# Optimization experiments

Hardware: AMD Instinct MI355X
Metric: run time of the kernel (lower is better)

The kernel has to match this reference:

```python
import jax, jax.numpy as jnp
import numpy as np

N_NODES = 10000
N_EDGES = 320000
NODE_F = 64
EDGE_F = 32
H = 256
L = 6
HEADS = 8
OUT = H // HEADS
N_GRAPHS = 16
NEG_SLOPE = 0.2  # PyG GATConv leaky_relu slope


def setup_inputs() -> dict:
    key = jax.random.key(0)
    ks = jax.random.split(key, 32)
    s = 0.05
    f32 = jnp.float32
    inp = {}
    inp["x"] = jax.random.normal(ks[0], (N_NODES, NODE_F), f32)
    inp["edge_index"] = jax.random.randint(ks[1], (2, N_EDGES), 0, N_NODES)
    inp["edge_attr"] = jax.random.normal(ks[2], (N_EDGES, EDGE_F), f32)
    inp["batch"] = jnp.sort(jax.random.randint(ks[3], (N_NODES,), 0, N_GRAPHS))
    # embeddings
    inp["node_w"] = jax.random.normal(ks[4], (H, NODE_F), f32) * s
    inp["node_b"] = jnp.zeros((H,), f32)
    inp["edge_emb_w"] = jax.random.normal(ks[5], (H, EDGE_F), f32) * s
    inp["edge_emb_b"] = jnp.zeros((H,), f32)
    # stacked GATConv params (shared lin for src/dst since in_channels is int)
    inp["lin_w"] = jax.random.normal(ks[6], (L, H, H), f32) * s
    inp["att_src"] = jax.random.normal(ks[7], (L, HEADS, OUT), f32) * s
    inp["att_dst"] = jax.random.normal(ks[8], (L, HEADS, OUT), f32) * s
    inp["att_edge"] = jax.random.normal(ks[9], (L, HEADS, OUT), f32) * s
    inp["lin_edge_w"] = jax.random.normal(ks[10], (L, H, H), f32) * s
    inp["conv_b"] = jnp.zeros((L, H), f32)
    inp["ln_g"] = jnp.ones((L, H), f32)
    inp["ln_b"] = jnp.zeros((L, H), f32)
    # MLP heads: Linear(2H->H), Linear(H->H/2), Linear(H/2->3)
    inp["pw1"] = jax.random.normal(ks[11], (H, 2 * H), f32) * s
    inp["pb1"] = jnp.zeros((H,), f32)
    inp["pw2"] = jax.random.normal(ks[12], (H // 2, H), f32) * s
    inp["pb2"] = jnp.zeros((H // 2,), f32)
    inp["pw3"] = jax.random.normal(ks[13], (3, H // 2), f32) * s
    inp["pb3"] = jnp.zeros((3,), f32)
    inp["mw1"] = jax.random.normal(ks[14], (H, 2 * H), f32) * s
    inp["mb1"] = jnp.zeros((H,), f32)
    inp["mw2"] = jax.random.normal(ks[15], (H // 2, H), f32) * s
    inp["mb2"] = jnp.zeros((H // 2,), f32)
    inp["mw3"] = jax.random.normal(ks[16], (3, H // 2), f32) * s
    inp["mb3"] = jnp.zeros((3,), f32)
    return inp


def _ln(x, g, b):
    mu = jnp.mean(x, -1, keepdims=True)
    var = jnp.mean(jnp.square(x - mu), -1, keepdims=True)
    return g * (x - mu) * jax.lax.rsqrt(var + 1e-5) + b


def _mlp(z, w1, b1, w2, b2, w3, b3):
    h = jax.nn.gelu(z @ w1.T + b1, approximate=False)
    h = jax.nn.gelu(h @ w2.T + b2, approximate=False)
    return jax.nn.sigmoid(h @ w3.T + b3)


def _gnn_forward(x, edge_attr, src, dst, batch,
                 node_w, node_b, edge_emb_w, edge_emb_b,
                 lin_w, att_src, att_dst, att_edge, lin_edge_w, conv_b,
                 ln_g, ln_b,
                 pw1, pb1, pw2, pb2, pw3, pb3,
                 mw1, mb1, mw2, mb2, mw3, mb3):
    h = x @ node_w.T + node_b                       # [N, H]
    ea = edge_attr @ edge_emb_w.T + edge_emb_b      # [E, H]
    # PyG add_self_loops(fill_value='mean'): loop attr = mean of incoming edge attrs
    cnt = jax.ops.segment_sum(jnp.ones((N_EDGES,), h.dtype), dst, N_NODES)
    loop_attr = jax.ops.segment_sum(ea, dst, N_NODES) / jnp.maximum(cnt, 1.0)[:, None]
    ea_full = jnp.concatenate([ea, loop_attr], 0)   # [E+N, H]
    loops = jnp.arange(N_NODES, dtype=src.dtype)
    src_f = jnp.concatenate([src, loops])
    dst_f = jnp.concatenate([dst, loops])
    for i in range(L):
        x_in = h
        xw = (h @ lin_w[i].T).reshape(N_NODES, HEADS, OUT)
        eap = (ea_full @ lin_edge_w[i].T).reshape(-1, HEADS, OUT)
        a_src = jnp.sum(xw * att_src[i], -1)        # [N, heads]
        a_dst = jnp.sum(xw * att_dst[i], -1)
        alpha = a_src[src_f] + a_dst[dst_f] + jnp.sum(eap * att_edge[i], -1)  # [E+N, heads]
        alpha = jnp.where(alpha > 0, alpha, NEG_SLOPE * alpha)
        amax = jax.ops.segment_max(alpha, dst_f, N_NODES)
        e = jnp.exp(alpha - amax[dst_f])
        denom = jax.ops.segment_sum(e, dst_f, N_NODES)
        w = e / (denom[dst_f] + 1e-16)
        msg = xw[src_f] * w[:, :, None]             # [E+N, heads, out]
        hi = jax.ops.segment_sum(msg, dst_f, N_NODES).reshape(N_NODES, H) + conv_b[i]
        hi = jax.nn.gelu(_ln(hi, ln_g[i], ln_b[i]), approximate=False)
        h = hi + x_in if i > 0 else hi
    sums = jax.ops.segment_sum(h, batch, N_GRAPHS)  # [G, H]
    ncnt = jax.ops.segment_sum(jnp.ones((N_NODES,), h.dtype), batch, N_GRAPHS)
    mean = sums / jnp.maximum(ncnt, 1.0)[:, None]
    xg = jnp.concatenate([mean, sums], 1)           # [G, 2H]
    params = _mlp(xg, pw1, pb1, pw2, pb2, pw3, pb3)
    metrics = _mlp(xg, mw1, mb1, mw2, mb2, mw3, mb3)
    return params, metrics


def reference(x, edge_index, edge_attr, batch,
              node_w, node_b, edge_emb_w, edge_emb_b,
              lin_w, att_src, att_dst, att_edge, lin_edge_w, conv_b,
              ln_g, ln_b,
              pw1, pb1, pw2, pb2, pw3, pb3,
              mw1, mb1, mw2, mb2, mw3, mb3):
    return _gnn_forward(x, edge_attr, edge_index[0], edge_index[1], batch,
                        node_w, node_b, edge_emb_w, edge_emb_b,
                        lin_w, att_src, att_dst, att_edge, lin_edge_w, conv_b,
                        ln_g, ln_b,
                        pw1, pb1, pw2, pb2, pw3, pb3,
                        mw1, mb1, mw2, mb2, mw3, mb3)
```

## Files before the change

### kernel.cpp

```cpp
#include <hip/hip_runtime.h>
#include <math.h>

#define NN 10000
#define NE 320000
#define NODE_F 64
#define EDGE_F 32
#define HDIM 256
#define HEADS 8
#define LAYERS 6
#define NG 16
#define NOUT 48
#define LOG2E 1.4426950408889634f

typedef __attribute__((ext_vector_type(8))) short short8;
typedef __attribute__((ext_vector_type(4))) float float4v;
typedef __attribute__((ext_vector_type(2))) float floatx2;

__global__ void scan_kernel(const int* __restrict__ cnt, int* __restrict__ row_ptr,
                            int* __restrict__ pos) {
    __shared__ int wsum[16];
    __shared__ int woff[16];
    int t = threadIdx.x;
    int lane = t & 63, wid = t >> 6;
    const int chunk = 10;
    int lo = t * chunk;
    int loc[10];
    int s = 0;
    #pragma unroll
    for (int k = 0; k < 10; ++k) {
        int i = lo + k;
        int v = (i < NN) ? cnt[i] : 0;
        loc[k] = v;
        s += v;
    }
    int inc = s;
    #pragma unroll
    for (int off = 1; off < 64; off <<= 1) {
        int v = __shfl_up(inc, off, 64);
        if (lane >= off) inc += v;
    }
    if (lane == 63) wsum[wid] = inc;
    __syncthreads();
    if (t < 16) {
        int inc2 = wsum[t];
        #pragma unroll
        for (int off = 1; off < 16; off <<= 1) {
            int u = __shfl_up(inc2, off, 16);
            if (t >= off) inc2 += u;
        }
        woff[t] = inc2;
    }
    __syncthreads();
    int base = inc - s + (wid ? woff[wid - 1] : 0);
    #pragma unroll
    for (int k = 0; k < 10; ++k) {
        int i = lo + k;
        if (i < NN) {
            row_ptr[i] = base;
            pos[i] = base;
            base += loc[k];
        }
    }
    if (t == 1023) row_ptr[NN] = woff[15];
}

__global__ void scatter_kernel(const int* __restrict__ src, const int* __restrict__ dst,
                               int* __restrict__ pos, int2* __restrict__ csr_se) {
    int e = blockIdx.x * 256 + threadIdx.x;
    if (e >= NE) return;
    int d = dst[e];
    int idx = atomicAdd(&pos[d], 1);
    csr_se[idx] = make_int2(src[e], e);
}

__device__ __forceinline__ ushort f2bf(float f) {
    union { float f; unsigned u; } v; v.f = f;
    unsigned u = v.u;
    return (ushort)((u + 0x7fffu + ((u >> 16) & 1u)) >> 16);
}
__device__ __forceinline__ float bf2f(ushort b) {
    union { unsigned u; float f; } v; v.u = ((unsigned)b) << 16; return v.f;
}

__global__ __launch_bounds__(256) void prep_kernel(const float* __restrict__ att_edge,
                                                   const float* __restrict__ lin_edge_w,
                                                   const float* __restrict__ eew,
                                                   const float* __restrict__ eeb,
                                                   ushort* __restrict__ webbf,
                                                   float* __restrict__ bebuf) {
    int ih = blockIdx.x;
    int i = ih >> 3, h = ih & 7;
    __shared__ float vsh[HDIM];
    int t = threadIdx.x;
    float s = 0.f;
    const float* ae = att_edge + ih * 32;
    const float* lw = lin_edge_w + ((size_t)i * HDIM + h * 32) * HDIM + t;
    #pragma unroll
    for (int o = 0; o < 32; ++o) s += ae[o] * lw[(size_t)o * HDIM];
    vsh[t] = s;
    __syncthreads();
    if (t < EDGE_F) {
        float acc = 0.f;
        for (int k = 0; k < HDIM; ++k) acc += vsh[k] * eew[k * EDGE_F + t];
        webbf[ih * EDGE_F + t] = f2bf(acc * LOG2E);
    } else if (t == EDGE_F) {
        float acc = 0.f;
        for (int k = 0; k < HDIM; ++k) acc += vsh[k] * eeb[k];
        bebuf[ih] = acc * LOG2E;
    }
}

__global__ __launch_bounds__(64) void fold0_kernel(const float* __restrict__ lin_w,
                                                   const float* __restrict__ node_w,
                                                   const float* __restrict__ node_b,
                                                   ushort* __restrict__ w0p,
                                                   float* __restrict__ b0p) {
    int j = blockIdx.x, f = threadIdx.x;
    const float* wr = lin_w + (size_t)j * HDIM;
    float acc = 0.f, accb = 0.f;
    for (int k = 0; k < HDIM; ++k) acc += wr[k] * node_w[k * NODE_F + f];
    #pragma unroll
    for (int m = 0; m < 4; ++m) {
        int k = f + 64 * m;
        accb += wr[k] * node_b[k];
    }
    w0p[j * NODE_F + f] = f2bf(acc);
    #pragma unroll
    for (int off = 32; off >= 1; off >>= 1) accb += __shfl_xor(accb, off, 64);
    if (f == 0) b0p[j] = accb;
}

__global__ __launch_bounds__(256) void preE_kernel(const float* __restrict__ edge_attr,
                                                   const ushort* __restrict__ web,
                                                   const float* __restrict__ be,
                                                   unsigned char* __restrict__ preE8,
                                                   const int* __restrict__ dst,
                                                   int* __restrict__ cnt) {
    int t = threadIdx.x;
    if (t < 64) atomicAdd(&cnt[dst[blockIdx.x * 64 + t]], 1);
    int wv = t >> 6, l = t & 63;
    int base = blockIdx.x * 64 + wv * 16;
    int m = l & 15, kq = (l >> 4) * 8;
    const float* ar = edge_attr + (size_t)(base + m) * EDGE_F + kq;
    float4 a0 = *(const float4*)(ar);
    float4 a1 = *(const float4*)(ar + 4);
    short8 afrag;
    afrag[0] = (short)f2bf(a0.x); afrag[1] = (short)f2bf(a0.y);
    afrag[2] = (short)f2bf(a0.z); afrag[3] = (short)f2bf(a0.w);
    afrag[4] = (short)f2bf(a1.x); afrag[5] = (short)f2bf(a1.y);
    afrag[6] = (short)f2bf(a1.z); afrag[7] = (short)f2bf(a1.w);
    float4v zero = {0.f, 0.f, 0.f, 0.f};
    float4v acc[3];
    #pragma unroll
    for (int ct = 0; ct < 3; ++ct) {
        short8 bfrag = *(const short8*)(web + (size_t)(ct * 16 + m) * EDGE_F + kq);
        acc[ct] = __builtin_amdgcn_mfma_f32_16x16x32_bf16(afrag, bfrag, zero, 0, 0, 0);
    }
    #pragma unroll
    for (int ct = 0; ct < 3; ++ct) {
        int oc = ct * 16 + m;
        int li = oc >> 3, hh = oc & 7;
        float bv = be[oc];
        #pragma unroll
        for (int r = 0; r < 4; ++r) {
            int row = (l >> 4) * 4 + r;
            float v = acc[ct][r] + bv;
            int pk8 = __builtin_amdgcn_cvt_pk_fp8_f32(v, v, 0, false);
            preE8[(size_t)li * NE * 8 + (size_t)(base + row) * 8 + hh] =
                (unsigned char)(pk8 & 0xff);
        }
    }
}

__global__ void tobf_all_kernel(const float* __restrict__ lin_w,
                                const float* __restrict__ x, ushort* __restrict__ wbhi,
                                ushort* __restrict__ xhi) {
    const int N1 = LAYERS * HDIM * HDIM;
    const int N2 = N1 + NN * NODE_F;
    int i = blockIdx.x * 256 + threadIdx.x;
    if (i < N1) wbhi[i] = f2bf(lin_w[i]);
    else if (i < N2) xhi[i - N1] = f2bf(x[i - N1]);
}

__global__ __launch_bounds__(128) void gemm_bf1(const ushort* __restrict__ Ah,
                                                const ushort* __restrict__ Bh,
                                                const float* __restrict__ bias,
                                                unsigned char* __restrict__ Cf8,
                                                const float* __restrict__ att_s,
                                                const float* __restrict__ att_d,
                                                float* __restrict__ a_src,
                                                float* __restrict__ a_dst,
                                                int N, int K) {
    __shared__ ushort sAh[64][40], sBh[64][40];
    int nb = blockIdx.y * 64, jb = blockIdx.x * 64;
    int t = threadIdx.x, w = t >> 6, l = t & 63;
    int srow = t >> 1, sq = (t & 1) * 16;
    int fr = l & 15, fq = (l >> 4) * 8;
    float4v acc[2][4] = {};
    for (int kt = 0; kt < K; kt += 32) {
        int gr = nb + srow;
        short8 a0 = {0,0,0,0,0,0,0,0}, a1 = {0,0,0,0,0,0,0,0};
        if (gr < N) {
            const short8* pa = (const short8*)(Ah + (size_t)gr * K + kt + sq);
            a0 = pa[0]; a1 = pa[1];
        }
        *(short8*)&sAh[srow][sq] = a0; *(short8*)&sAh[srow][sq + 8] = a1;
        const short8* pb = (const short8*)(Bh + (size_t)(jb + srow) * K + kt + sq);
        short8 b0 = pb[0], b1 = pb[1];
        *(short8*)&sBh[srow][sq] = b0; *(short8*)&sBh[srow][sq + 8] = b1;
        __syncthreads();
        short8 bh[4];
        #pragma unroll
        for (int nt = 0; nt < 4; ++nt)
            bh[nt] = *(const short8*)&sBh[nt * 16 + fr][fq];
        #pragma unroll
        for (int mt = 0; mt < 2; ++mt) {
            short8 ah = *(const short8*)&sAh[w * 32 + mt * 16 + fr][fq];
            #pragma unroll
            for (int nt = 0; nt < 4; ++nt)
                acc[mt][nt] = __builtin_amdgcn_mfma_f32_16x16x32_bf16(ah, bh[nt], acc[mt][nt], 0, 0, 0);
        }
        __syncthreads();
    }
    if (bias) {
        #pragma unroll
        for (int nt = 0; nt < 4; ++nt) {
            float bv = bias[jb + nt * 16 + fr];
            #pragma unroll
            for (int mt = 0; mt < 2; ++mt)
                #pragma unroll
                for (int r = 0; r < 4; ++r) acc[mt][nt][r] += bv;
        }
    }
    #pragma unroll
    for (int mt = 0; mt < 2; ++mt) {
        #pragma unroll
        for (int nt = 0; nt < 4; ++nt) {
            int col = jb + nt * 16 + fr;
            #pragma unroll
            for (int r = 0; r < 4; ++r) {
                int row = nb + w * 32 + mt * 16 + (l >> 4) * 4 + r;
                if (row < N) {
                    float v = acc[mt][nt][r];
                    int pk8 = __builtin_amdgcn_cvt_pk_fp8_f32(v, v, 0, false);
                    Cf8[(size_t)row * HDIM + col] = (unsigned char)(pk8 & 0xff);
                }
            }
        }
    }
    {
        int head0 = jb >> 5;
        float cs[4], cd[4];
        #pragma unroll
        for (int nt = 0; nt < 4; ++nt) {
            cs[nt] = att_s[jb + nt * 16 + fr] * LOG2E;
            cd[nt] = att_d[jb + nt * 16 + fr] * LOG2E;
        }
        #pragma unroll
        for (int mt = 0; mt < 2; ++mt) {
            #pragma unroll
            for (int r = 0; r < 4; ++r) {
                float s0 = acc[mt][0][r] * cs[0] + acc[mt][1][r] * cs[1];
                float s1 = acc[mt][2][r] * cs[2] + acc[mt][3][r] * cs[3];
                float d0 = acc[mt][0][r] * cd[0] + acc[mt][1][r] * cd[1];
                float d1 = acc[mt][2][r] * cd[2] + acc[mt][3][r] * cd[3];
                #pragma unroll
                for (int off = 8; off >= 1; off >>= 1) {
                    s0 += __shfl_xor(s0, off, 16);
                    s1 += __shfl_xor(s1, off, 16);
                    d0 += __shfl_xor(d0, off, 16);
                    d1 += __shfl_xor(d1, off, 16);
                }
                if (fr == 0) {
                    int row = nb + w * 32 + mt * 16 + (l >> 4) * 4 + r;
                    if (row < N) {
                        a_src[row * 8 + head0]     = s0;
                        a_src[row * 8 + head0 + 1] = s1;
                        a_dst[row * 8 + head0]     = d0;
                        a_dst[row * 8 + head0 + 1] = d1;
                    }
                }
            }
        }
    }
}

__device__ __forceinline__ float gelu_exact(float x) {
    return 0.5f * x * (1.f + erff(x * 0.70710678118654752f));
}

__global__ __launch_bounds__(128) void node_kernel(const unsigned char* __restrict__ xwf8,
                                                  const unsigned char* __restrict__ pb,
                                                  const float* __restrict__ a_src,
                                                  const float* __restrict__ a_dst,
                                                  const int* __restrict__ row_ptr,
                                                  const int2* __restrict__ csr_se,
                                                  const ushort* __restrict__ hp,
                                                  ushort* __restrict__ hout,
                                                  const float* __restrict__ cb,
                                                  const float* __restrict__ lg,
                                                  const float* __restrict__ lb, int first) {
    __shared__ float red[6][128];
    int t = threadIdx.x;
    int wv = t >> 6, l = t & 63;
    int n = blockIdx.x;
    int start = row_ptr[n], end = row_ptr[n + 1];
    int hc = l >> 3;
    int hc8 = l & 56;
    int jj = l & 7;
    float adnh = a_dst[n * 8 + hc];
    const unsigned char* xb = xwf8 + 4 * l;

    float den = 0.f, acc[4] = {0.f, 0.f, 0.f, 0.f};
    float psum = 0.f;
    for (int idx = start + wv * 8; idx < end; idx += 16) {
        int myi = idx + jj;
        bool valid = myi < end;
        int2 se = valid ? csr_se[myi] : make_int2(n, 0);
        int snj[8];
        #pragma unroll
        for (int j = 0; j < 8; ++j) snj[j] = __shfl(se.x, hc8 + j, 64);
        unsigned g[8];
        #pragma unroll
        for (int j = 0; j < 8; ++j) g[j] = *(const unsigned*)(xb + (size_t)snj[j] * HDIM);
        float w_t = 0.f;
        if (valid) {
            unsigned pu = pb[(size_t)se.y * 8 + hc];
            floatx2 pd = __builtin_amdgcn_cvt_pk_f32_fp8(pu, false);
            float p_t = pd.x;
            float a_t = a_src[(size_t)se.x * 8 + hc] + adnh + p_t;
            w_t = exp2f(fminf(fmaxf(a_t, 0.2f * a_t), 57.7f));
            psum += p_t;
        }
        #pragma unroll
        for (int j = 0; j < 8; ++j) {
            float wj = __shfl(w_t, hc8 + j, 64);
            floatx2 lo = __builtin_amdgcn_cvt_pk_f32_fp8(g[j], false);
            floatx2 hi = __builtin_amdgcn_cvt_pk_f32_fp8(g[j], true);
            den += wj;
            acc[0] += wj * lo.x;
            acc[1] += wj * lo.y;
            acc[2] += wj * hi.x;
            acc[3] += wj * hi.y;
        }
    }
    #pragma unroll
    for (int off = 1; off < 8; off <<= 1) psum += __shfl_xor(psum, off, 64);
    red[0][t] = den; red[1][t] = acc[0]; red[2][t] = acc[1];
    red[3][t] = acc[2]; red[4][t] = acc[3]; red[5][t] = psum;
    __syncthreads();
    int ot = t ^ 64;
    den += red[0][ot]; acc[0] += red[1][ot]; acc[1] += red[2][ot];
    acc[2] += red[3][ot]; acc[3] += red[4][ot]; psum += red[5][ot];

    int deg = end - start;
    float preLv = deg > 0 ? psum / (float)deg : 0.f;
    {
        float al = a_src[n * 8 + hc] + adnh + preLv;
        al = fminf(fmaxf(al, 0.2f * al), 57.7f);
        float wself = exp2f(al);
        den += wself;
        unsigned gs = *(const unsigned*)(xb + (size_t)n * HDIM);
        floatx2 lo = __builtin_amdgcn_cvt_pk_f32_fp8(gs, false);
        floatx2 hi = __builtin_amdgcn_cvt_pk_f32_fp8(gs, true);
        acc[0] += wself * lo.x;
        acc[1] += wself * lo.y;
        acc[2] += wself * hi.x;
        acc[3] += wself * hi.y;
    }
    float4 cb4 = *(const float4*)(cb + 4 * l);
    float invh = 1.f / (den + 1e-16f);
    acc[0] = acc[0] * invh + cb4.x;
    acc[1] = acc[1] * invh + cb4.y;
    acc[2] = acc[2] * invh + cb4.z;
    acc[3] = acc[3] * invh + cb4.w;

    float part = acc[0] + acc[1] + acc[2] + acc[3];
    #pragma unroll
    for (int off = 32; off >= 1; off >>= 1) part += __shfl_xor(part, off, 64);
    float mu = part * (1.f / 256.f);
    float p2 = 0.f;
    #pragma unroll
    for (int j = 0; j < 4; ++j) {
        float d = acc[j] - mu;
        p2 += d * d;
    }
    #pragma unroll
    for (int off = 32; off >= 1; off >>= 1) p2 += __shfl_xor(p2, off, 64);
    float rstd = rsqrtf(p2 * (1.f / 256.f) + 1e-5f);

    if (wv == 0) {
        float4 lg4 = *(const float4*)(lg + 4 * l);
        float4 lb4 = *(const float4*)(lb + 4 * l);
        float o4[4];
        float lgv[4] = {lg4.x, lg4.y, lg4.z, lg4.w};
        float lbv[4] = {lb4.x, lb4.y, lb4.z, lb4.w};
        float hpv[4] = {0.f, 0.f, 0.f, 0.f};
        if (!first) {
            uint2 ph = *(const uint2*)(hp + (size_t)n * HDIM + 4 * l);
            hpv[0] = bf2f((ushort)(ph.x & 0xffff));
            hpv[1] = bf2f((ushort)(ph.x >> 16));
            hpv[2] = bf2f((ushort)(ph.y & 0xffff));
            hpv[3] = bf2f((ushort)(ph.y >> 16));
        }
        #pragma unroll
        for (int j = 0; j < 4; ++j) {
            float y = (acc[j] - mu) * rstd * lgv[j] + lbv[j];
            o4[j] = gelu_exact(y) + hpv[j];
        }
        uint2 po;
        po.x = (unsigned)f2bf(o4[0]) | ((unsigned)f2bf(o4[1]) << 16);
        po.y = (unsigned)f2bf(o4[2]) | ((unsigned)f2bf(o4[3]) << 16);
        *(uint2*)(hout + (size_t)n * HDIM + 4 * l) = po;
    }
}

__global__ __launch_bounds__(256) void graph_sum_kernel(const ushort* __restrict__ h,
                                                        const int* __restrict__ batch,
                                                        float* __restrict__ sums) {
    int t = threadIdx.x;
    int n0 = blockIdx.x * 64;
    int n1 = min(NN, n0 + 64);
    float acc = 0.f;
    int cur = batch[n0];
    for (int n = n0; n < n1; ++n) {
        int b = batch[n];
        if (b != cur) {
            atomicAdd(&sums[cur * HDIM + t], acc);
            acc = 0.f;
            cur = b;
        }
        acc += bf2f(h[(size_t)n * HDIM + t]);
    }
    atomicAdd(&sums[cur * HDIM + t], acc);
}

__device__ __forceinline__ int lower_bound_dev(const int* a, int n, int v) {
    int lo = 0, hi = n;
    while (lo < hi) {
        int mid = (lo + hi) >> 1;
        if (a[mid] < v) lo = mid + 1; else hi = mid;
    }
    return lo;
}

__global__ __launch_bounds__(256) void mlp_kernel(const float* __restrict__ sums,
                                                  const int* __restrict__ batch,
                                                  const float* __restrict__ pw1,
                                                  const float* __restrict__ pb1,
                                                  const float* __restrict__ pw2,
                                                  const float* __restrict__ pb2,
                                                  const float* __restrict__ pw3,
                                                  const float* __restrict__ pb3,
                                                  const float* __restrict__ mw1,
                                                  const float* __restrict__ mb1,
                                                  const float* __restrict__ mw2,
                                                  const float* __restrict__ mb2,
                                                  const float* __restrict__ mw3,
                                                  const float* __restrict__ mb3,
                                                  float* __restrict__ out) {
    int g = blockIdx.x, which = blockIdx.y;
    const float* w1 = which ? mw1 : pw1; const float* b1 = which ? mb1 : pb1;
    const float* w2 = which ? mw2 : pw2; const float* b2 = which ? mb2 : pb2;
    const float* w3 = which ? mw3 : pw3; const float* b3 = which ? mb3 : pb3;
    __shared__ float xg[512];
    __shared__ float h1[256];
    __shared__ float h2[128];
    __shared__ float cinv_s;
    int t = threadIdx.x;
    if (t == 0) {
        int s0 = lower_bound_dev(batch, NN, g), s1 = lower_bound_dev(batch, NN, g + 1);
        cinv_s = 1.f / fmaxf((float)(s1 - s0), 1.f);
    }
    __syncthreads();
    float sv = sums[g * HDIM + t];
    xg[t] = sv * cinv_s;
    xg[256 + t] = sv;
    __syncthreads();
    {
        const float* wr = w1 + (size_t)t * 512;
        float acc = 0.f;
        #pragma unroll 8
        for (int k = 0; k < 512; k += 4) {
            float4 wv = *(const float4*)(wr + k);
            acc += wv.x * xg[k] + wv.y * xg[k + 1] + wv.z * xg[k + 2] + wv.w * xg[k + 3];
        }
        h1[t] = gelu_exact(acc + b1[t]);
    }
    __syncthreads();
    {
        int row = t >> 1, hf = t & 1;
        const float* wr = w2 + (size_t)row * 256 + hf * 128;
        const float* hx = h1 + hf * 128;
        float acc = 0.f;
        #pragma unroll 8
        for (int k = 0; k < 128; k += 4) {
            float4 wv = *(const float4*)(wr + k);
            acc += wv.x * hx[k] + wv.y * hx[k + 1] + wv.z * hx[k + 2] + wv.w * hx[k + 3];
        }
        acc += __shfl_xor(acc, 1, 64);
        if (hf == 0) h2[row] = gelu_exact(acc + b2[row]);
    }
    __syncthreads();
    if (t < 64) {
        float v0 = h2[t], v1 = h2[64 + t];
        #pragma unroll
        for (int o = 0; o < 3; ++o) {
            float p = w3[o * 128 + t] * v0 + w3[o * 128 + 64 + t] * v1;
            #pragma unroll
            for (int off = 32; off >= 1; off >>= 1) p += __shfl_xor(p, off, 64);
            if (t == 0) out[which * (NG * 3) + g * 3 + o] = 1.f / (1.f + expf(-(p + b3[o])));
        }
    }
}

extern "C" void kernel_launch(void* const* d_in, const int* in_sizes, int n_in, void* d_out,
                              int out_size, void* d_ws, size_t ws_size, hipStream_t stream) {
    const float* x         = (const float*)d_in[0];
    const int*   ei        = (const int*)d_in[1];
    const int*   src       = ei;
    const int*   dst       = ei + NE;
    const float* edge_attr = (const float*)d_in[2];
    const int*   batch     = (const int*)d_in[3];
    const float* node_w    = (const float*)d_in[4];
    const float* node_b    = (const float*)d_in[5];
    const float* eew       = (const float*)d_in[6];
    const float* eeb       = (const float*)d_in[7];
    const float* lin_w     = (const float*)d_in[8];
    const float* att_src   = (const float*)d_in[9];
    const float* att_dst   = (const float*)d_in[10];
    const float* att_edge  = (const float*)d_in[11];
    const float* lin_edge_w= (const float*)d_in[12];
    const float* conv_b    = (const float*)d_in[13];
    const float* ln_g      = (const float*)d_in[14];
    const float* ln_b      = (const float*)d_in[15];
    const float* pw1 = (const float*)d_in[16]; const float* pb1 = (const float*)d_in[17];
    const float* pw2 = (const float*)d_in[18]; const float* pb2 = (const float*)d_in[19];
    const float* pw3 = (const float*)d_in[20]; const float* pb3 = (const float*)d_in[21];
    const float* mw1 = (const float*)d_in[22]; const float* mb1 = (const float*)d_in[23];
    const float* mw2 = (const float*)d_in[24]; const float* mb2 = (const float*)d_in[25];
    const float* mw3 = (const float*)d_in[26]; const float* mb3 = (const float*)d_in[27];
    float* out = (float*)d_out;

    float* wsf = (float*)d_ws;
    float* a_src     = wsf; wsf += (size_t)NN * HEADS;
    float* a_dst     = wsf; wsf += (size_t)NN * HEADS;
    float* bebuf     = wsf; wsf += 64;
    float* b0p       = wsf; wsf += HDIM;
    ushort* ubuf = (ushort*)wsf;
    ushort* webbf = ubuf; ubuf += (size_t)NOUT * EDGE_F;
    ushort* hb0  = ubuf; ubuf += (size_t)NN * HDIM;
    ushort* hb1  = ubuf; ubuf += (size_t)NN * HDIM;
    ushort* wbhi = ubuf; ubuf += (size_t)LAYERS * HDIM * HDIM;
    ushort* xhi  = ubuf; ubuf += (size_t)NN * NODE_F;
    ushort* w0p  = ubuf; ubuf += (size_t)HDIM * NODE_F;
    unsigned char* cbuf = (unsigned char*)ubuf;
    unsigned char* preE8 = cbuf; cbuf += (size_t)NE * NOUT;
    unsigned char* xwf8  = cbuf; cbuf += (size_t)NN * HDIM;
    cbuf += ((size_t)cbuf & 7) ? (8 - ((size_t)cbuf & 7)) : 0;
    int* ibuf    = (int*)cbuf;
    int* cnt     = ibuf; ibuf += NN + 16;
    float* sums  = (float*)ibuf; ibuf += NG * HDIM;
    int* row_ptr = ibuf; ibuf += NN + 16;
    int* pos     = ibuf; ibuf += NN + 16;
    int2* csr_se = (int2*)ibuf; ibuf += 2 * NE;

    hipMemsetAsync(cnt, 0, (NN + 16 + NG * HDIM) * sizeof(int), stream);

    prep_kernel<<<LAYERS * HEADS, 256, 0, stream>>>(att_edge, lin_edge_w, eew, eeb, webbf, bebuf);
    preE_kernel<<<NE / 64, 256, 0, stream>>>(edge_attr, webbf, bebuf, preE8, dst, cnt);

    scan_kernel<<<1, 1024, 0, stream>>>(cnt, row_ptr, pos);
    scatter_kernel<<<(NE + 255) / 256, 256, 0, stream>>>(src, dst, pos, csr_se);

    {
        const int total = LAYERS * HDIM * HDIM + NN * NODE_F;
        tobf_all_kernel<<<(total + 255) / 256, 256, 0, stream>>>(lin_w, x, wbhi, xhi);
    }
    fold0_kernel<<<HDIM, 64, 0, stream>>>(lin_w, node_w, node_b, w0p, b0p);

    ushort* hb[2] = {hb0, hb1};
    for (int i = 0; i < LAYERS; ++i) {
        dim3 grid(HDIM / 64, (NN + 63) / 64);
        const ushort* Ain = (i == 0) ? xhi : hb[(i - 1) & 1];
        const ushort* Bin = (i == 0) ? w0p : wbhi + (size_t)i * HDIM * HDIM;
        int Kin = (i == 0) ? NODE_F : HDIM;
        const float* bias = (i == 0) ? b0p : nullptr;
        gemm_bf1<<<grid, 128, 0, stream>>>(Ain, Bin, bias, xwf8,
                                           att_src + i * HEADS * 32, att_dst + i * HEADS * 32,
                                           a_src, a_dst, NN, Kin);
        node_kernel<<<NN, 128, 0, stream>>>(
            xwf8, preE8 + (size_t)i * NE * 8, a_src, a_dst,
            row_ptr, csr_se, (i == 0) ? nullptr : hb[(i - 1) & 1], hb[i & 1],
            conv_b + i * HDIM, ln_g + i * HDIM, ln_b + i * HDIM, i == 0 ? 1 : 0);
    }

    graph_sum_kernel<<<(NN + 63) / 64, 256, 0, stream>>>(hb[(LAYERS - 1) & 1], batch, sums);
    {
        dim3 gm(NG, 2);
        mlp_kernel<<<gm, 256, 0, stream>>>(sums, batch, pw1, pb1, pw2, pb2, pw3, pb3,
                                           mw1, mb1, mw2, mb2, mw3, mb3, out);
    }
}
```

Before: 464.0 us.

## Merge setup kernels into one launch and enlarge GEMM row tile to 128

Three one-time preprocessing kernels (edge attention fold, layer-0 weight fold, bf16 conversion) are merged into a single launch that dispatches on block index, with a grid-stride loop for the conversion part. This removes two kernel launches and lets the independent setup work run concurrently. The per-layer GEMM now uses 256 threads and 128-row A tiles, halving the number of row blocks and reusing each B tile across more rows. The cost is fewer blocks for the 10000-row GEMM (79x4), which may leave some CUs idle.

Result: no change. 457.3 us (-1.5%).

```diff
diff --git a/kernel.cpp b/kernel.cpp
--- a/kernel.cpp
+++ b/kernel.cpp
@@ -82,52 +82,68 @@
     union { unsigned u; float f; } v; v.u = ((unsigned)b) << 16; return v.f;
 }
 
-__global__ __launch_bounds__(256) void prep_kernel(const float* __restrict__ att_edge,
-                                                   const float* __restrict__ lin_edge_w,
-                                                   const float* __restrict__ eew,
-                                                   const float* __restrict__ eeb,
-                                                   ushort* __restrict__ webbf,
-                                                   float* __restrict__ bebuf) {
-    int ih = blockIdx.x;
-    int i = ih >> 3, h = ih & 7;
+__global__ __launch_bounds__(256) void setup_kernel(const float* __restrict__ att_edge,
+                                                    const float* __restrict__ lin_edge_w,
+                                                    const float* __restrict__ eew,
+                                                    const float* __restrict__ eeb,
+                                                    ushort* __restrict__ webbf,
+                                                    float* __restrict__ bebuf,
+                                                    const float* __restrict__ lin_w,
+                                                    const float* __restrict__ node_w,
+                                                    const float* __restrict__ node_b,
+                                                    ushort* __restrict__ w0p,
+                                                    float* __restrict__ b0p,
+                                                    const float* __restrict__ x,
+                                                    ushort* __restrict__ wbhi,
+                                                    ushort* __restrict__ xhi,
+                                                    int nblk) {
     __shared__ float vsh[HDIM];
     int t = threadIdx.x;
-    float s = 0.f;
-    const float* ae = att_edge + ih * 32;
-    const float* lw = lin_edge_w + ((size_t)i * HDIM + h * 32) * HDIM + t;
-    #pragma unroll
-    for (int o = 0; o < 32; ++o) s += ae[o] * lw[(size_t)o * HDIM];
-    vsh[t] = s;
-    __syncthreads();
-    if (t < EDGE_F) {
-        float acc = 0.f;
-        for (int k = 0; k < HDIM; ++k) acc += vsh[k] * eew[k * EDGE_F + t];
-        webbf[ih * EDGE_F + t] = f2bf(acc * LOG2E);
-    } else if (t == EDGE_F) {
-        float acc = 0.f;
-        for (int k = 0; k < HDIM; ++k) acc += vsh[k] * eeb[k];
-        bebuf[ih] = acc * LOG2E;
-    }
-}
-
-__global__ __launch_bounds__(64) void fold0_kernel(const float* __restrict__ lin_w,
-                                                   const float* __restrict__ node_w,
-                                                   const float* __restrict__ node_b,
-                                                   ushort* __restrict__ w0p,
-                                                   float* __restrict__ b0p) {
-    int j = blockIdx.x, f = threadIdx.x;
-    const float* wr = lin_w + (size_t)j * HDIM;
-    float acc = 0.f, accb = 0.f;
-    for (int k = 0; k < HDIM; ++k) acc += wr[k] * node_w[k * NODE_F + f];
-    #pragma unroll
-    for (int m = 0; m < 4; ++m) {
-        int k = f + 64 * m;
-        accb += wr[k] * node_b[k];
-    }
-    w0p[j * NODE_F + f] = f2bf(acc);
-    #pragma unroll
-    for (int off = 32; off >= 1; off >>= 1) accb += __shfl_xor(accb, off, 64);
-    if (f == 0) b0p[j] = accb;
+    int b = blockIdx.x;
+    if (b < LAYERS * HEADS) {
+        int ih = b;
+        int i = ih >> 3, h = ih & 7;
+        float s = 0.f;
+        const float* ae = att_edge + ih * 32;
+        const float* lw = lin_edge_w + ((size_t)i * HDIM + h * 32) * HDIM + t;
+        #pragma unroll
+        for (int o = 0; o < 32; ++o) s += ae[o] * lw[(size_t)o * HDIM];
+        vsh[t] = s;
+        __syncthreads();
+        if (t < EDGE_F) {
+            float acc = 0.f;
+            for (int k = 0; k < HDIM; ++k) acc += vsh[k] * eew[k * EDGE_F + t];
+            webbf[ih * EDGE_F + t] = f2bf(acc * LOG2E);
+        } else if (t == EDGE_F) {
+            float acc = 0.f;
+            for (int k = 0; k < HDIM; ++k) acc += vsh[k] * eeb[k];
+            bebuf[ih] = acc * LOG2E;
+        }
+    } else if (b < LAYERS * HEADS + HDIM) {
+        if (t < 64) {
+            int j = b - LAYERS * HEADS, f = t;
+            const float* wr = lin_w + (size_t)j * HDIM;
+            float acc = 0.f, accb = 0.f;
+            for (int k = 0; k < HDIM; ++k) acc += wr[k] * node_w[k * NODE_F + f];
+            #pragma unroll
+            for (int m = 0; m < 4; ++m) {
+                int k = f + 64 * m;
+                accb += wr[k] * node_b[k];
+            }
+            w0p[j * NODE_F + f] = f2bf(acc);
+            #pragma unroll
+            for (int off = 32; off >= 1; off >>= 1) accb += __shfl_xor(accb, off, 64);
+            if (f == 0) b0p[j] = accb;
+        }
+    } else {
+        const int N1 = LAYERS * HDIM * HDIM;
+        const int N2 = N1 + NN * NODE_F;
+        int base = LAYERS * HEADS + HDIM;
+        for (int i = (b - base) * 256 + t; i < N2; i += (nblk - base) * 256) {
+            if (i < N1) wbhi[i] = f2bf(lin_w[i]);
+            else xhi[i - N1] = f2bf(x[i - N1]);
+        }
+    }
 }
 
 __global__ __launch_bounds__(256) void preE_kernel(const float* __restrict__ edge_attr,
@@ -172,17 +188,7 @@
     }
 }
 
-__global__ void tobf_all_kernel(const float* __restrict__ lin_w,
-                                const float* __restrict__ x, ushort* __restrict__ wbhi,
-                                ushort* __restrict__ xhi) {
-    const int N1 = LAYERS * HDIM * HDIM;
-    const int N2 = N1 + NN * NODE_F;
-    int i = blockIdx.x * 256 + threadIdx.x;
-    if (i < N1) wbhi[i] = f2bf(lin_w[i]);
-    else if (i < N2) xhi[i - N1] = f2bf(x[i - N1]);
-}
-
-__global__ __launch_bounds__(128) void gemm_bf1(const ushort* __restrict__ Ah,
+__global__ __launch_bounds__(256) void gemm_bf1(const ushort* __restrict__ Ah,
                                                 const ushort* __restrict__ Bh,
                                                 const float* __restrict__ bias,
                                                 unsigned char* __restrict__ Cf8,
@@ -191,23 +197,24 @@
                                                 float* __restrict__ a_src,
                                                 float* __restrict__ a_dst,
                                                 int N, int K) {
-    __shared__ ushort sAh[64][40], sBh[64][40];
-    int nb = blockIdx.y * 64, jb = blockIdx.x * 64;
+    __shared__ ushort sAh[128][40];
+    __shared__ ushort sBh[64][40];
+    int nb = blockIdx.y * 128, jb = blockIdx.x * 64;
     int t = threadIdx.x, w = t >> 6, l = t & 63;
-    int srow = t >> 1, sq = (t & 1) * 16;
+    int arow = t >> 1, asq = (t & 1) * 16;
+    int brow = t >> 2, bsq = (t & 3) * 8;
     int fr = l & 15, fq = (l >> 4) * 8;
     float4v acc[2][4] = {};
     for (int kt = 0; kt < K; kt += 32) {
-        int gr = nb + srow;
+        int gr = nb + arow;
         short8 a0 = {0,0,0,0,0,0,0,0}, a1 = {0,0,0,0,0,0,0,0};
         if (gr < N) {
-            const short8* pa = (const short8*)(Ah + (size_t)gr * K + kt + sq);
+            const short8* pa = (const short8*)(Ah + (size_t)gr * K + kt + asq);
             a0 = pa[0]; a1 = pa[1];
         }
-        *(short8*)&sAh[srow][sq] = a0; *(short8*)&sAh[srow][sq + 8] = a1;
-        const short8* pb = (const short8*)(Bh + (size_t)(jb + srow) * K + kt + sq);
-        short8 b0 = pb[0], b1 = pb[1];
-        *(short8*)&sBh[srow][sq] = b0; *(short8*)&sBh[srow][sq + 8] = b1;
+        *(short8*)&sAh[arow][asq] = a0; *(short8*)&sAh[arow][asq + 8] = a1;
+        short8 b0 = *(const short8*)(Bh + (size_t)(jb + brow) * K + kt + bsq);
+        *(short8*)&sBh[brow][bsq] = b0;
         __syncthreads();
         short8 bh[4];
         #pragma unroll
@@ -567,26 +574,23 @@
 
     hipMemsetAsync(cnt, 0, (NN + 16 + NG * HDIM) * sizeof(int), stream);
 
-    prep_kernel<<<LAYERS * HEADS, 256, 0, stream>>>(att_edge, lin_edge_w, eew, eeb, webbf, bebuf);
+    const int SETUP_BLK = LAYERS * HEADS + HDIM + 1024;
+    setup_kernel<<<SETUP_BLK, 256, 0, stream>>>(att_edge, lin_edge_w, eew, eeb, webbf, bebuf,
+                                                lin_w, node_w, node_b, w0p, b0p,
+                                                x, wbhi, xhi, SETUP_BLK);
     preE_kernel<<<NE / 64, 256, 0, stream>>>(edge_attr, webbf, bebuf, preE8, dst, cnt);
 
     scan_kernel<<<1, 1024, 0, stream>>>(cnt, row_ptr, pos);
     scatter_kernel<<<(NE + 255) / 256, 256, 0, stream>>>(src, dst, pos, csr_se);
 
-    {
-        const int total = LAYERS * HDIM * HDIM + NN * NODE_F;
-        tobf_all_kernel<<<(total + 255) / 256, 256, 0, stream>>>(lin_w, x, wbhi, xhi);
-    }
-    fold0_kernel<<<HDIM, 64, 0, stream>>>(lin_w, node_w, node_b, w0p, b0p);
-
     ushort* hb[2] = {hb0, hb1};
     for (int i = 0; i < LAYERS; ++i) {
-        dim3 grid(HDIM / 64, (NN + 63) / 64);
+        dim3 grid(HDIM / 64, (NN + 127) / 128);
         const ushort* Ain = (i == 0) ? xhi : hb[(i - 1) & 1];
         const ushort* Bin = (i == 0) ? w0p : wbhi + (size_t)i * HDIM * HDIM;
         int Kin = (i == 0) ? NODE_F : HDIM;
         const float* bias = (i == 0) ? b0p : nullptr;
-        gemm_bf1<<<grid, 128, 0, stream>>>(Ain, Bin, bias, xwf8,
+        gemm_bf1<<<grid, 256, 0, stream>>>(Ain, Bin, bias, xwf8,
                                            att_src + i * HEADS * 32, att_dst + i * HEADS * 32,
                                            a_src, a_dst, NN, Kin);
         node_kernel<<<NN, 128, 0, stream>>>(
```
